# Performance work log

Hardware: AMD Instinct MI355X
Metric: run time of the kernel (lower is better)

Reference implementation:

```python
import jax, jax.numpy as jnp
import numpy as np

THRESH = 0.9   # config['thresh_cnn']
R = 2          # config['radius'] -> maxpool kernel 2R+1=5, stride 1, padding R


def setup_inputs() -> dict:
    key = jax.random.key(0)
    # [B=1, C=1, D=64, H=512, W=512]
    pred_vol = jax.random.uniform(key, (1, 1, 64, 512, 512), dtype=jnp.float32)
    return {"pred_vol": pred_vol}


def reference(pred_vol):
    # threshold: keep values > thresh, else 0
    pred_thresh = jnp.where(pred_vol > THRESH, pred_vol, 0.0)
    # 3D max-pool, kernel 2R+1, stride 1, padding R (torch pads with -inf for maxpool)
    k = 2 * R + 1
    mp = jax.lax.reduce_window(
        pred_thresh, -jnp.inf, jax.lax.max,
        window_dimensions=(1, 1, k, k, k),
        window_strides=(1, 1, 1, 1, 1),
        padding=[(0, 0), (0, 0), (R, R), (R, R), (R, R)],
    )
    # keep only strict local maxima of the thresholded volume
    conf_vol = jnp.where((mp > 0.0) & (mp == pred_thresh), mp, 0.0)
    return jnp.squeeze(conf_vol)  # [D, H, W] dense peak confidence map
```

## Files before the change

kernel.cpp:

```cpp
#include <hip/hip_runtime.h>
#include <stdint.h>


#define THRESH 0.9f

constexpr int D = 64, H = 512, W = 512;
constexpr int HW = H * W;
constexpr int TW = 64;
constexpr int TH = 16;
constexpr int DCHUNK = 8;
constexpr int HALO = 2;
constexpr int LROWS = TH + 2 * HALO;
constexpr int RAWQ  = TW / 4 + 2;
constexpr int NQ = LROWS * RAWQ;
constexpr int QCAP = 512;
constexpr int NS = DCHUNK + 2 * HALO;

typedef float floatx4 __attribute__((ext_vector_type(4)));
using gu32p = const __attribute__((address_space(1))) uint32_t*;
using lu32p = __attribute__((address_space(3))) uint32_t*;

__device__ __forceinline__ float4 max4(float4 a, float4 b) {
    return make_float4(fmaxf(a.x, b.x), fmaxf(a.y, b.y),
                       fmaxf(a.z, b.z), fmaxf(a.w, b.w));
}

__device__ __forceinline__ float4 wmax5s(float f2, float f3, float4 b,
                                         float f8, float f9) {
    const float f4 = b.x, f5 = b.y, f6 = b.z, f7 = b.w;
    const float m45 = fmaxf(f4, f5);
    const float m56 = fmaxf(f5, f6);
    const float m345 = fmaxf(f3, m45);
    const float m456 = fmaxf(f4, m56);
    const float m567 = fmaxf(m56, f7);
    const float m678 = fmaxf(fmaxf(f6, f7), f8);
    float4 r;
    r.x = fmaxf(fmaxf(f2, f6), m345);
    r.y = fmaxf(fmaxf(f3, f7), m456);
    r.z = fmaxf(fmaxf(f4, f8), m567);
    r.w = fmaxf(fmaxf(f5, f9), m678);
    return r;
}

__global__ __launch_bounds__(256)
__attribute__((amdgpu_num_vgpr(64)))
void peak3d_kernel(const float* __restrict__ in, float* __restrict__ out) {
    __shared__ float4 raw[2][QCAP];

    const int tx = threadIdx.x;
    const int ty = threadIdx.y;
    const int tid = ty * 16 + tx;

    const int w0 = blockIdx.x * TW;
    const int h0 = blockIdx.y * TH;
    const int d0 = blockIdx.z * DCHUNK;

    const int q0 = tid;
    const int q1c = min(tid + 256, NQ - 1);
    const int r0 = q0 / RAWQ, c0 = q0 % RAWQ;
    const int r1 = q1c / RAWQ, c1 = q1c % RAWQ;
    const int gh0 = min(max(h0 + r0 - HALO, 0), H - 1);
    const int gw0 = min(max(w0 + 4 * c0 - 4, 0), W - 4);
    const int gh1 = min(max(h0 + r1 - HALO, 0), H - 1);
    const int gw1 = min(max(w0 + 4 * c1 - 4, 0), W - 4);
    const int off0 = gh0 * W + gw0;
    const int off1 = gh1 * W + gw1;

    const int rbase = ty * RAWQ + tx + 1;
    const bool isL = (tx == 0), isR = (tx == 15);
    const bool edgeW = (isL && w0 == 0) || (isR && w0 == W - TW);
    const int hbase = (ty * RAWQ + (isL ? 0 : RAWQ - 1)) * 2 + (isL ? 1 : 0);

    const float4 zero4 = make_float4(0.f, 0.f, 0.f, 0.f);
    float4 win[5];
    float4 cen[2];
#pragma unroll
    for (int k = 0; k < 5; ++k) win[k] = zero4;
    cen[0] = zero4; cen[1] = zero4;

    auto stage = [&](int t) {
        const int dd = min(max(d0 - HALO + t, 0), D - 1);
        const float* sp = in + dd * HW;
        float4* ldsb = &raw[t & 1][0];
        __builtin_amdgcn_global_load_lds((gu32p)(sp + off0),
                                         (lu32p)(ldsb + tid), 16, 0, 0);
        __builtin_amdgcn_global_load_lds((gu32p)(sp + off1),
                                         (lu32p)(ldsb + tid + 256), 16, 0, 0);
    };

    stage(0);
    asm volatile("s_waitcnt vmcnt(0) lgkmcnt(0)" ::: "memory");
    __builtin_amdgcn_s_barrier();

#pragma unroll
    for (int t = 0; t < NS; ++t) {
        const int buf = t & 1;

        if (t + 1 < NS) stage(t + 1);

        const float4* bp = &raw[buf][0];
        const float4 r0q = bp[rbase + 0 * RAWQ];
        const float4 r1q = bp[rbase + 1 * RAWQ];
        const float4 r2q = bp[rbase + 2 * RAWQ];
        const float4 r3q = bp[rbase + 3 * RAWQ];
        const float4 r4q = bp[rbase + 4 * RAWQ];
        const float4 hv = max4(max4(max4(r0q, r1q), max4(r3q, r4q)), r2q);

        float2 h = make_float2(0.f, 0.f);
        if (isL || isR) {
            const float2* hp = reinterpret_cast<const float2*>(bp);
            const float2 e0 = hp[hbase + 0 * RAWQ * 2];
            const float2 e1 = hp[hbase + 1 * RAWQ * 2];
            const float2 e2 = hp[hbase + 2 * RAWQ * 2];
            const float2 e3 = hp[hbase + 3 * RAWQ * 2];
            const float2 e4 = hp[hbase + 4 * RAWQ * 2];
            h.x = fmaxf(fmaxf(fmaxf(e0.x, e1.x), fmaxf(e3.x, e4.x)), e2.x);
            h.y = fmaxf(fmaxf(fmaxf(e0.y, e1.y), fmaxf(e3.y, e4.y)), e2.y);
            if (edgeW) { h.x = 0.f; h.y = 0.f; }
        }

        float f2 = __shfl_up(hv.z, 1);
        float f3 = __shfl_up(hv.w, 1);
        float f8 = __shfl_down(hv.x, 1);
        float f9 = __shfl_down(hv.y, 1);
        if (isL) { f2 = h.x; f3 = h.y; }
        if (isR) { f8 = h.x; f9 = h.y; }

        win[t % 5] = wmax5s(f2, f3, hv, f8, f9);

        if (t >= 4) {
            const int dout = d0 + (t - 4);
            const float4 mp = max4(max4(max4(win[0], win[1]),
                                        max4(win[2], win[3])), win[4]);
            const float4 c = cen[t & 1];
            floatx4 res;
            res.x = (c.x > THRESH && mp.x == c.x) ? c.x : 0.f;
            res.y = (c.y > THRESH && mp.y == c.y) ? c.y : 0.f;
            res.z = (c.z > THRESH && mp.z == c.z) ? c.z : 0.f;
            res.w = (c.w > THRESH && mp.w == c.w) ? c.w : 0.f;
            floatx4* op = reinterpret_cast<floatx4*>(
                out + (size_t)(dout * HW + (h0 + ty) * W + (w0 + 4 * tx)));
            __builtin_nontemporal_store(res, op);
        }
        cen[t & 1] = r2q;

        if (t + 1 < NS) {
            if (t >= 4) {
                asm volatile("s_waitcnt vmcnt(1) lgkmcnt(0)" ::: "memory");
            } else {
                asm volatile("s_waitcnt vmcnt(0) lgkmcnt(0)" ::: "memory");
            }
            __builtin_amdgcn_s_barrier();
        }
    }
}

extern "C" void kernel_launch(void* const* d_in, const int* in_sizes, int n_in,
                              void* d_out, int out_size, void* d_ws, size_t ws_size,
                              hipStream_t stream) {
    const float* in = (const float*)d_in[0];
    float* out = (float*)d_out;
    dim3 grid(W / TW, H / TH, D / DCHUNK);
    dim3 block(16, 16, 1);
    hipLaunchKernelGGL(peak3d_kernel, grid, block, 0, stream, in, out);
}
```

Baseline: 118.5 us.

## Give each wave its own LDS tile and drop block barriers

Splits the 16-row block tile into four independent 4-row wave tiles. Each wave stages its own 8-row halo region into a private double-buffered LDS slice with three async global-to-LDS loads per lane, and synchronises only through per-wave vmcnt waits instead of block-wide s_barrier. This removes barrier stalls between waves and lets them run out of lockstep. In exchange, redundant halo row loads rise from 20 rows per 16 output rows to 8 rows per 4, which adds cache and global read traffic.

Measured after the change: 121.9 us. 2.9% more time.

```diff
diff --git a/kernel.cpp b/kernel.cpp
--- a/kernel.cpp
+++ b/kernel.cpp
@@ -7,13 +7,14 @@
 constexpr int D = 64, H = 512, W = 512;
 constexpr int HW = H * W;
 constexpr int TW = 64;
-constexpr int TH = 16;
+constexpr int WH = 4;
+constexpr int NWAVES = 4;
 constexpr int DCHUNK = 8;
 constexpr int HALO = 2;
-constexpr int LROWS = TH + 2 * HALO;
-constexpr int RAWQ  = TW / 4 + 2;
-constexpr int NQ = LROWS * RAWQ;
-constexpr int QCAP = 512;
+constexpr int SROWS = WH + 2 * HALO;
+constexpr int RAWQ = TW / 4 + 2;
+constexpr int NQ = SROWS * RAWQ;
+constexpr int SLOTS = 192;
 constexpr int NS = DCHUNK + 2 * HALO;
 
 typedef float floatx4 __attribute__((ext_vector_type(4)));
@@ -45,31 +46,33 @@
 __global__ __launch_bounds__(256)
 __attribute__((amdgpu_num_vgpr(64)))
 void peak3d_kernel(const float* __restrict__ in, float* __restrict__ out) {
-    __shared__ float4 raw[2][QCAP];
+    __shared__ float4 raw[NWAVES][2][SLOTS];
 
-    const int tx = threadIdx.x;
-    const int ty = threadIdx.y;
-    const int tid = ty * 16 + tx;
+    const int tid = threadIdx.y * 16 + threadIdx.x;
+    const int wid = tid >> 6;
+    const int lane = tid & 63;
+    const int tx = lane & 15;
+    const int tyw = lane >> 4;
 
     const int w0 = blockIdx.x * TW;
-    const int h0 = blockIdx.y * TH;
+    const int hb = blockIdx.y * (WH * NWAVES) + wid * WH;
     const int d0 = blockIdx.z * DCHUNK;
 
-    const int q0 = tid;
-    const int q1c = min(tid + 256, NQ - 1);
-    const int r0 = q0 / RAWQ, c0 = q0 % RAWQ;
-    const int r1 = q1c / RAWQ, c1 = q1c % RAWQ;
-    const int gh0 = min(max(h0 + r0 - HALO, 0), H - 1);
-    const int gw0 = min(max(w0 + 4 * c0 - 4, 0), W - 4);
-    const int gh1 = min(max(h0 + r1 - HALO, 0), H - 1);
-    const int gw1 = min(max(w0 + 4 * c1 - 4, 0), W - 4);
-    const int off0 = gh0 * W + gw0;
-    const int off1 = gh1 * W + gw1;
+    int off0, off1, off2;
+#pragma unroll
+    for (int i = 0; i < 3; ++i) {
+        int s = min(i * 64 + lane, NQ - 1);
+        const int r = s / RAWQ, c = s % RAWQ;
+        const int gh = min(max(hb + r - HALO, 0), H - 1);
+        const int gw = min(max(w0 + 4 * c - 4, 0), W - 4);
+        const int o = gh * W + gw;
+        if (i == 0) off0 = o; else if (i == 1) off1 = o; else off2 = o;
+    }
 
-    const int rbase = ty * RAWQ + tx + 1;
+    const int rbase = tyw * RAWQ + tx + 1;
     const bool isL = (tx == 0), isR = (tx == 15);
     const bool edgeW = (isL && w0 == 0) || (isR && w0 == W - TW);
-    const int hbase = (ty * RAWQ + (isL ? 0 : RAWQ - 1)) * 2 + (isL ? 1 : 0);
+    const int hbase = (tyw * RAWQ + (isL ? 0 : RAWQ - 1)) * 2 + (isL ? 1 : 0);
 
     const float4 zero4 = make_float4(0.f, 0.f, 0.f, 0.f);
     float4 win[5];
@@ -81,16 +84,16 @@
     auto stage = [&](int t) {
         const int dd = min(max(d0 - HALO + t, 0), D - 1);
         const float* sp = in + dd * HW;
-        float4* ldsb = &raw[t & 1][0];
+        float4* ldsb = &raw[wid][t & 1][0];
         __builtin_amdgcn_global_load_lds((gu32p)(sp + off0),
-                                         (lu32p)(ldsb + tid), 16, 0, 0);
+                                         (lu32p)(ldsb + 0),   16, 0, 0);
         __builtin_amdgcn_global_load_lds((gu32p)(sp + off1),
-                                         (lu32p)(ldsb + tid + 256), 16, 0, 0);
+                                         (lu32p)(ldsb + 64),  16, 0, 0);
+        __builtin_amdgcn_global_load_lds((gu32p)(sp + off2),
+                                         (lu32p)(ldsb + 128), 16, 0, 0);
     };
 
     stage(0);
-    asm volatile("s_waitcnt vmcnt(0) lgkmcnt(0)" ::: "memory");
-    __builtin_amdgcn_s_barrier();
 
 #pragma unroll
     for (int t = 0; t < NS; ++t) {
@@ -98,7 +101,15 @@
 
         if (t + 1 < NS) stage(t + 1);
 
-        const float4* bp = &raw[buf][0];
+        if (t == NS - 1) {
+            asm volatile("s_waitcnt vmcnt(1)" ::: "memory");
+        } else if (t >= 5) {
+            asm volatile("s_waitcnt vmcnt(4)" ::: "memory");
+        } else {
+            asm volatile("s_waitcnt vmcnt(3)" ::: "memory");
+        }
+
+        const float4* bp = &raw[wid][buf][0];
         const float4 r0q = bp[rbase + 0 * RAWQ];
         const float4 r1q = bp[rbase + 1 * RAWQ];
         const float4 r2q = bp[rbase + 2 * RAWQ];
@@ -139,19 +150,10 @@
             res.z = (c.z > THRESH && mp.z == c.z) ? c.z : 0.f;
             res.w = (c.w > THRESH && mp.w == c.w) ? c.w : 0.f;
             floatx4* op = reinterpret_cast<floatx4*>(
-                out + (size_t)(dout * HW + (h0 + ty) * W + (w0 + 4 * tx)));
+                out + (size_t)(dout * HW + (hb + tyw) * W + (w0 + 4 * tx)));
             __builtin_nontemporal_store(res, op);
         }
         cen[t & 1] = r2q;
-
-        if (t + 1 < NS) {
-            if (t >= 4) {
-                asm volatile("s_waitcnt vmcnt(1) lgkmcnt(0)" ::: "memory");
-            } else {
-                asm volatile("s_waitcnt vmcnt(0) lgkmcnt(0)" ::: "memory");
-            }
-            __builtin_amdgcn_s_barrier();
-        }
     }
 }
 
@@ -160,7 +162,7 @@
                               hipStream_t stream) {
     const float* in = (const float*)d_in[0];
     float* out = (float*)d_out;
-    dim3 grid(W / TW, H / TH, D / DCHUNK);
+    dim3 grid(W / TW, H / (WH * NWAVES), D / DCHUNK);
     dim3 block(16, 16, 1);
     hipLaunchKernelGGL(peak3d_kernel, grid, block, 0, stream, in, out);
 }
```

## Replace LDS staging with direct global loads per thread

Applied to the files above, without the earlier changes.

Removes the double-buffered LDS staging (global_load_lds plus barriers) and has each thread load its five rows and the halo columns straight from global memory, relying on cache for reuse across threads. The VGPR cap is raised to 128 so the loads can be held and issued in flight. This drops the barriers and LDS traffic, but roughly quintuples global/L1 load instructions, and the higher register budget may lower occupancy.

New measurement: 124.9 us. +5.4%, slower.

```diff
diff --git a/kernel.cpp b/kernel.cpp
--- a/kernel.cpp
+++ b/kernel.cpp
@@ -1,5 +1,4 @@
 #include <hip/hip_runtime.h>
-#include <stdint.h>
 
 
 #define THRESH 0.9f
@@ -10,15 +9,9 @@
 constexpr int TH = 16;
 constexpr int DCHUNK = 8;
 constexpr int HALO = 2;
-constexpr int LROWS = TH + 2 * HALO;
-constexpr int RAWQ  = TW / 4 + 2;
-constexpr int NQ = LROWS * RAWQ;
-constexpr int QCAP = 512;
 constexpr int NS = DCHUNK + 2 * HALO;
 
 typedef float floatx4 __attribute__((ext_vector_type(4)));
-using gu32p = const __attribute__((address_space(1))) uint32_t*;
-using lu32p = __attribute__((address_space(3))) uint32_t*;
 
 __device__ __forceinline__ float4 max4(float4 a, float4 b) {
     return make_float4(fmaxf(a.x, b.x), fmaxf(a.y, b.y),
@@ -43,33 +36,29 @@
 }
 
 __global__ __launch_bounds__(256)
-__attribute__((amdgpu_num_vgpr(64)))
+__attribute__((amdgpu_num_vgpr(128)))
 void peak3d_kernel(const float* __restrict__ in, float* __restrict__ out) {
-    __shared__ float4 raw[2][QCAP];
-
     const int tx = threadIdx.x;
-    const int ty = threadIdx.y;
-    const int tid = ty * 16 + tx;
+    const int tyb = threadIdx.y;
 
     const int w0 = blockIdx.x * TW;
     const int h0 = blockIdx.y * TH;
     const int d0 = blockIdx.z * DCHUNK;
 
-    const int q0 = tid;
-    const int q1c = min(tid + 256, NQ - 1);
-    const int r0 = q0 / RAWQ, c0 = q0 % RAWQ;
-    const int r1 = q1c / RAWQ, c1 = q1c % RAWQ;
-    const int gh0 = min(max(h0 + r0 - HALO, 0), H - 1);
-    const int gw0 = min(max(w0 + 4 * c0 - 4, 0), W - 4);
-    const int gh1 = min(max(h0 + r1 - HALO, 0), H - 1);
-    const int gw1 = min(max(w0 + 4 * c1 - 4, 0), W - 4);
-    const int off0 = gh0 * W + gw0;
-    const int off1 = gh1 * W + gw1;
+    const int ty = h0 + tyb;
+    const int col = w0 + 4 * tx;
 
-    const int rbase = ty * RAWQ + tx + 1;
     const bool isL = (tx == 0), isR = (tx == 15);
     const bool edgeW = (isL && w0 == 0) || (isR && w0 == W - TW);
-    const int hbase = (ty * RAWQ + (isL ? 0 : RAWQ - 1)) * 2 + (isL ? 1 : 0);
+    const int hcol = isL ? max(w0 - 2, 0) : min(w0 + TW, W - 2);
+
+    int off[5], hoff[5];
+#pragma unroll
+    for (int k = 0; k < 5; ++k) {
+        const int gh = min(max(ty + k - HALO, 0), H - 1);
+        off[k] = gh * W + col;
+        hoff[k] = gh * W + hcol;
+    }
 
     const float4 zero4 = make_float4(0.f, 0.f, 0.f, 0.f);
     float4 win[5];
@@ -78,46 +67,29 @@
     for (int k = 0; k < 5; ++k) win[k] = zero4;
     cen[0] = zero4; cen[1] = zero4;
 
-    auto stage = [&](int t) {
-        const int dd = min(max(d0 - HALO + t, 0), D - 1);
-        const float* sp = in + dd * HW;
-        float4* ldsb = &raw[t & 1][0];
-        __builtin_amdgcn_global_load_lds((gu32p)(sp + off0),
-                                         (lu32p)(ldsb + tid), 16, 0, 0);
-        __builtin_amdgcn_global_load_lds((gu32p)(sp + off1),
-                                         (lu32p)(ldsb + tid + 256), 16, 0, 0);
-    };
-
-    stage(0);
-    asm volatile("s_waitcnt vmcnt(0) lgkmcnt(0)" ::: "memory");
-    __builtin_amdgcn_s_barrier();
-
 #pragma unroll
     for (int t = 0; t < NS; ++t) {
-        const int buf = t & 1;
+        const float* sb = in + min(max(d0 - HALO + t, 0), D - 1) * HW;
 
-        if (t + 1 < NS) stage(t + 1);
-
-        const float4* bp = &raw[buf][0];
-        const float4 r0q = bp[rbase + 0 * RAWQ];
-        const float4 r1q = bp[rbase + 1 * RAWQ];
-        const float4 r2q = bp[rbase + 2 * RAWQ];
-        const float4 r3q = bp[rbase + 3 * RAWQ];
-        const float4 r4q = bp[rbase + 4 * RAWQ];
-        const float4 hv = max4(max4(max4(r0q, r1q), max4(r3q, r4q)), r2q);
+        const float4 r0 = *reinterpret_cast<const float4*>(sb + off[0]);
+        const float4 r1 = *reinterpret_cast<const float4*>(sb + off[1]);
+        const float4 r2 = *reinterpret_cast<const float4*>(sb + off[2]);
+        const float4 r3 = *reinterpret_cast<const float4*>(sb + off[3]);
+        const float4 r4 = *reinterpret_cast<const float4*>(sb + off[4]);
 
         float2 h = make_float2(0.f, 0.f);
         if (isL || isR) {
-            const float2* hp = reinterpret_cast<const float2*>(bp);
-            const float2 e0 = hp[hbase + 0 * RAWQ * 2];
-            const float2 e1 = hp[hbase + 1 * RAWQ * 2];
-            const float2 e2 = hp[hbase + 2 * RAWQ * 2];
-            const float2 e3 = hp[hbase + 3 * RAWQ * 2];
-            const float2 e4 = hp[hbase + 4 * RAWQ * 2];
+            const float2 e0 = *reinterpret_cast<const float2*>(sb + hoff[0]);
+            const float2 e1 = *reinterpret_cast<const float2*>(sb + hoff[1]);
+            const float2 e2 = *reinterpret_cast<const float2*>(sb + hoff[2]);
+            const float2 e3 = *reinterpret_cast<const float2*>(sb + hoff[3]);
+            const float2 e4 = *reinterpret_cast<const float2*>(sb + hoff[4]);
             h.x = fmaxf(fmaxf(fmaxf(e0.x, e1.x), fmaxf(e3.x, e4.x)), e2.x);
             h.y = fmaxf(fmaxf(fmaxf(e0.y, e1.y), fmaxf(e3.y, e4.y)), e2.y);
             if (edgeW) { h.x = 0.f; h.y = 0.f; }
         }
+
+        const float4 hv = max4(max4(max4(r0, r1), max4(r3, r4)), r2);
 
         float f2 = __shfl_up(hv.z, 1);
         float f3 = __shfl_up(hv.w, 1);
@@ -139,19 +111,10 @@
             res.z = (c.z > THRESH && mp.z == c.z) ? c.z : 0.f;
             res.w = (c.w > THRESH && mp.w == c.w) ? c.w : 0.f;
             floatx4* op = reinterpret_cast<floatx4*>(
-                out + (size_t)(dout * HW + (h0 + ty) * W + (w0 + 4 * tx)));
+                out + (size_t)(dout * HW + ty * W + col));
             __builtin_nontemporal_store(res, op);
         }
-        cen[t & 1] = r2q;
-
-        if (t + 1 < NS) {
-            if (t >= 4) {
-                asm volatile("s_waitcnt vmcnt(1) lgkmcnt(0)" ::: "memory");
-            } else {
-                asm volatile("s_waitcnt vmcnt(0) lgkmcnt(0)" ::: "memory");
-            }
-            __builtin_amdgcn_s_barrier();
-        }
+        cen[t & 1] = r2;
     }
 }
 
```

## Deepen LDS staging to a 5-slot ring with 3-ahead prefetch and precise vmcnt waits

Applied to the files above, without the earlier changes.

Replaces the double-buffered LDS staging with a 5-deep ring buffer and issues global-to-LDS loads three depth slices ahead. Each step waits with a compile-time vmcnt that accounts for outstanding loads and stores. Only two of the four waves issue the second load, which trims the redundant clamped loads. DCHUNK is doubled, which halves the redundant halo depth slices per block but also halves the number of blocks in the grid. The LDS footprint grows to roughly 30KB, which may limit occupancy, and the hand-counted waits risk races if the counts are wrong.

After: 118.4 us. Within noise of the previous version (-0.0%).

```diff
diff --git a/kernel.cpp b/kernel.cpp
--- a/kernel.cpp
+++ b/kernel.cpp
@@ -1,5 +1,6 @@
 #include <hip/hip_runtime.h>
 #include <stdint.h>
+#include <utility>
 
 
 #define THRESH 0.9f
@@ -8,12 +9,13 @@
 constexpr int HW = H * W;
 constexpr int TW = 64;
 constexpr int TH = 16;
-constexpr int DCHUNK = 8;
+constexpr int DCHUNK = 16;
 constexpr int HALO = 2;
 constexpr int LROWS = TH + 2 * HALO;
-constexpr int RAWQ  = TW / 4 + 2;
+constexpr int RAWQ = TW / 4 + 2;
 constexpr int NQ = LROWS * RAWQ;
-constexpr int QCAP = 512;
+constexpr int SLOTS = 384;
+constexpr int DEPTH = 5;
 constexpr int NS = DCHUNK + 2 * HALO;
 
 typedef float floatx4 __attribute__((ext_vector_type(4)));
@@ -42,29 +44,47 @@
     return r;
 }
 
+template <int N>
+__device__ __forceinline__ void cwait() {
+    asm volatile("s_waitcnt vmcnt(%0)" :: "n"(N) : "memory");
+}
+
+template <typename F, int... I>
+__device__ __forceinline__ void static_for_impl(F&& f,
+                                                std::integer_sequence<int, I...>) {
+    (f(std::integral_constant<int, I>{}), ...);
+}
+template <int N, typename F>
+__device__ __forceinline__ void static_for(F&& f) {
+    static_for_impl(static_cast<F&&>(f), std::make_integer_sequence<int, N>{});
+}
+
 __global__ __launch_bounds__(256)
 __attribute__((amdgpu_num_vgpr(64)))
 void peak3d_kernel(const float* __restrict__ in, float* __restrict__ out) {
-    __shared__ float4 raw[2][QCAP];
+    __shared__ float4 raw[DEPTH][SLOTS];
 
-    const int tx = threadIdx.x;
-    const int ty = threadIdx.y;
-    const int tid = ty * 16 + tx;
+    const int tid = threadIdx.y * 16 + threadIdx.x;
+    const int wid = tid >> 6;
+    const int lane = tid & 63;
+    const int tx = tid & 15;
+    const int ty = tid >> 4;
 
     const int w0 = blockIdx.x * TW;
     const int h0 = blockIdx.y * TH;
     const int d0 = blockIdx.z * DCHUNK;
 
-    const int q0 = tid;
-    const int q1c = min(tid + 256, NQ - 1);
-    const int r0 = q0 / RAWQ, c0 = q0 % RAWQ;
-    const int r1 = q1c / RAWQ, c1 = q1c % RAWQ;
-    const int gh0 = min(max(h0 + r0 - HALO, 0), H - 1);
-    const int gw0 = min(max(w0 + 4 * c0 - 4, 0), W - 4);
-    const int gh1 = min(max(h0 + r1 - HALO, 0), H - 1);
-    const int gw1 = min(max(w0 + 4 * c1 - 4, 0), W - 4);
-    const int off0 = gh0 * W + gw0;
-    const int off1 = gh1 * W + gw1;
+    const bool hasB = (wid < 2);
+    const int sA = min(64 * wid + lane, NQ - 1);
+    const int sB = min(64 * (4 + wid) + lane, NQ - 1);
+    const int rA = sA / RAWQ, cA = sA % RAWQ;
+    const int rB = sB / RAWQ, cB = sB % RAWQ;
+    const int ghA = min(max(h0 + rA - HALO, 0), H - 1);
+    const int gwA = min(max(w0 + 4 * cA - 4, 0), W - 4);
+    const int ghB = min(max(h0 + rB - HALO, 0), H - 1);
+    const int gwB = min(max(w0 + 4 * cB - 4, 0), W - 4);
+    const int offA = ghA * W + gwA;
+    const int offB = ghB * W + gwB;
 
     const int rbase = ty * RAWQ + tx + 1;
     const bool isL = (tx == 0), isR = (tx == 15);
@@ -81,24 +101,29 @@
     auto stage = [&](int t) {
         const int dd = min(max(d0 - HALO + t, 0), D - 1);
         const float* sp = in + dd * HW;
-        float4* ldsb = &raw[t & 1][0];
-        __builtin_amdgcn_global_load_lds((gu32p)(sp + off0),
-                                         (lu32p)(ldsb + tid), 16, 0, 0);
-        __builtin_amdgcn_global_load_lds((gu32p)(sp + off1),
-                                         (lu32p)(ldsb + tid + 256), 16, 0, 0);
+        float4* ldsb = &raw[t % DEPTH][0];
+        __builtin_amdgcn_global_load_lds((gu32p)(sp + offA),
+                                         (lu32p)(ldsb + 64 * wid), 16, 0, 0);
+        if (hasB)
+            __builtin_amdgcn_global_load_lds((gu32p)(sp + offB),
+                                             (lu32p)(ldsb + 64 * (4 + wid)),
+                                             16, 0, 0);
     };
 
-    stage(0);
-    asm volatile("s_waitcnt vmcnt(0) lgkmcnt(0)" ::: "memory");
-    __builtin_amdgcn_s_barrier();
+    stage(0); stage(1); stage(2);
 
-#pragma unroll
-    for (int t = 0; t < NS; ++t) {
-        const int buf = t & 1;
+    static_for<NS>([&](auto tc) {
+        constexpr int t = decltype(tc)::value;
 
-        if (t + 1 < NS) stage(t + 1);
+        if (t + 3 < NS) stage(t + 3);
 
-        const float4* bp = &raw[buf][0];
+        constexpr int la = (t + 3 <= NS - 1) ? 3 : (NS - 1 - t);
+        constexpr int lo = (t - 3 > 4) ? (t - 3) : 4;
+        constexpr int sa = (t - 1 >= lo) ? (t - 1 - lo + 1) : 0;
+        if (hasB) cwait<2 * la + sa>(); else cwait<la + sa>();
+        asm volatile("s_barrier" ::: "memory");
+
+        const float4* bp = &raw[t % DEPTH][0];
         const float4 r0q = bp[rbase + 0 * RAWQ];
         const float4 r1q = bp[rbase + 1 * RAWQ];
         const float4 r2q = bp[rbase + 2 * RAWQ];
@@ -143,16 +168,7 @@
             __builtin_nontemporal_store(res, op);
         }
         cen[t & 1] = r2q;
-
-        if (t + 1 < NS) {
-            if (t >= 4) {
-                asm volatile("s_waitcnt vmcnt(1) lgkmcnt(0)" ::: "memory");
-            } else {
-                asm volatile("s_waitcnt vmcnt(0) lgkmcnt(0)" ::: "memory");
-            }
-            __builtin_amdgcn_s_barrier();
-        }
-    }
+    });
 }
 
 extern "C" void kernel_launch(void* const* d_in, const int* in_sizes, int n_in,
```
